# Kernel tuning notes

Measured on AMD Instinct MI355X. Metric: run time of the kernel, lower is better.

The kernel has to match this reference:

```python
import jax, jax.numpy as jnp
import numpy as np

B, C, W, H = 32, 256, 32, 32


def setup_inputs() -> dict:
    key = jax.random.key(0)
    ks = jax.random.split(key, 9)
    s = 1.0 / np.sqrt(C)
    return {
        "x": jax.random.normal(ks[0], (B, C, W, H), dtype=jnp.float32),
        "Wq": jax.random.normal(ks[1], (C, C), dtype=jnp.float32) * s,
        "bq": jax.random.normal(ks[2], (C,), dtype=jnp.float32) * 0.01,
        "Wk": jax.random.normal(ks[3], (C, C), dtype=jnp.float32) * s,
        "bk": jax.random.normal(ks[4], (C,), dtype=jnp.float32) * 0.01,
        "Wv": jax.random.normal(ks[5], (C, C), dtype=jnp.float32) * s,
        "bv": jax.random.normal(ks[6], (C,), dtype=jnp.float32) * 0.01,
        "rel_h": jax.random.normal(ks[7], (1, C, 1, H), dtype=jnp.float32),
        "rel_w": jax.random.normal(ks[8], (1, C, W, 1), dtype=jnp.float32),
    }


def reference(x, Wq, bq, Wk, bk, Wv, bv, rel_h, rel_w):
    b, c, w, h = x.shape
    n = w * h
    xf = x.reshape(b, c, n)  # [B, C, N]
    # 1x1 conv == channel-mixing matmul (out_ch 'o' from in_ch 'c')
    q = jnp.einsum('oc,bcn->bon', Wq, xf) + bq[None, :, None]
    k = jnp.einsum('oc,bcn->bon', Wk, xf) + bk[None, :, None]
    v = jnp.einsum('oc,bcn->bon', Wv, xf) + bv[None, :, None]
    # content-content: q^T k -> [B, N, N]
    content_content = jnp.einsum('bci,bcj->bij', q, k)
    # relative position bias: (rel_h + rel_w) broadcasts to [1, C, W, H]
    rel = (rel_h + rel_w).reshape(c, n)  # [C, N]
    content_position = jnp.einsum('cp,bcj->bpj', rel, q)  # [B, N, N]
    attention = jax.nn.softmax(content_content + content_position, axis=-1)
    # out[b,c,i] = sum_j v[b,c,j] * attention[b,i,j]
    out = jnp.einsum('bcj,bij->bci', v, attention)
    return out.reshape(b, c, w, h)
```

## Files before the change

### kernel.cpp

```cpp
#include <hip/hip_runtime.h>


#define NB 32
#define NC 256
#define NNN 1024

typedef _Float16 f16;
typedef __attribute__((ext_vector_type(8))) _Float16 half8;
typedef __attribute__((ext_vector_type(4))) float f32x4;
typedef __attribute__((ext_vector_type(4))) float float4v;

__device__ __forceinline__ f32x4 mfma16(half8 a, half8 b, f32x4 c) {
  return __builtin_amdgcn_mfma_f32_16x16x32_f16(a, b, c, 0, 0, 0);
}
__device__ __forceinline__ void gload16(const f16* g, f16* l) {
  __builtin_amdgcn_global_load_lds(
      (const __attribute__((address_space(1))) void*)g,
      (__attribute__((address_space(3))) void*)l, 16, 0, 0);
}

__global__ __launch_bounds__(256) void k_prep(
    const float* __restrict__ Wq, const float* __restrict__ Wk,
    const float* __restrict__ Wv, const float* __restrict__ relh,
    const float* __restrict__ relw, f16* __restrict__ Wh, f16* __restrict__ RT) {
  int bid = blockIdx.x, tid = threadIdx.x;
  if (bid < 192) {
    int base = (bid * 256 + tid) * 4;
    int w = base >> 16, j = base & 65535;
    const float* src = (w == 0) ? Wq : ((w == 1) ? Wk : Wv);
    float4v v = *(const float4v*)(src + j);
    Wh[base + 0] = (f16)v.x; Wh[base + 1] = (f16)v.y;
    Wh[base + 2] = (f16)v.z; Wh[base + 3] = (f16)v.w;
  } else {
    int n = bid - 192;
    int c = tid;
    RT[n * NC + c] = (f16)(relw[c * 32 + (n >> 5)] + relh[c * 32 + (n & 31)]);
  }
}

__global__ __launch_bounds__(256) void k_xpose(
    const float* __restrict__ x, f16* __restrict__ xT) {
  int bid = blockIdx.x;
  int nt = bid & 15, ct = (bid >> 4) & 3, b = bid >> 6;
  int c0 = ct << 6, n0 = nt << 6;
  __shared__ f16 T[64][72];
  int t = threadIdx.x;
  {
    int cl = t >> 2, n4 = (t & 3) << 4;
    const float* src = x + ((size_t)(b * NC + c0 + cl) << 10) + n0 + n4;
    float4v v0 = *(const float4v*)(src + 0);
    float4v v1 = *(const float4v*)(src + 4);
    float4v v2 = *(const float4v*)(src + 8);
    float4v v3 = *(const float4v*)(src + 12);
    f16* d = &T[cl][n4];
    d[0]=(f16)v0.x; d[1]=(f16)v0.y; d[2]=(f16)v0.z; d[3]=(f16)v0.w;
    d[4]=(f16)v1.x; d[5]=(f16)v1.y; d[6]=(f16)v1.z; d[7]=(f16)v1.w;
    d[8]=(f16)v2.x; d[9]=(f16)v2.y; d[10]=(f16)v2.z; d[11]=(f16)v2.w;
    d[12]=(f16)v3.x; d[13]=(f16)v3.y; d[14]=(f16)v3.z; d[15]=(f16)v3.w;
  }
  __syncthreads();
  {
    int nl = t >> 2, c16 = (t & 3) << 4;
    half8 h0, h1;
    #pragma unroll
    for (int u = 0; u < 8; ++u) h0[u] = T[c16 + u][nl];
    #pragma unroll
    for (int u = 0; u < 8; ++u) h1[u] = T[c16 + 8 + u][nl];
    f16* dst = xT + ((size_t)(b * NNN + n0 + nl) << 8) + c0 + c16;
    *(half8*)(dst) = h0;
    *(half8*)(dst + 8) = h1;
  }
}

__global__ __launch_bounds__(256, 2) void k_proj(
    const f16* __restrict__ xT, const f16* __restrict__ Wh,
    const float* __restrict__ bq, const float* __restrict__ bk,
    const float* __restrict__ bv,
    f16* __restrict__ KQ, f16* __restrict__ V) {
  int b = blockIdx.x >> 4;
  int n0 = (blockIdx.x & 15) << 6;
  int tid = threadIdx.x;
  int wave = tid >> 6, lane = tid & 63;
  int lq = lane & 15, g = lane >> 4;
  int ow = wave << 6;
  const f16* xTb = xT + ((size_t)(b * NNN + n0) << 8);

  __shared__ f16 XS[64][256];
  __shared__ f16 BB[18432];

  {
    int li = lane & 31;
    #pragma unroll
    for (int q2 = 0; q2 < 8; ++q2) {
      int r2 = wave * 16 + q2 * 2;
      int r = r2 + (lane >> 5);
      int slot = (li & 0x10) | ((li ^ (r & 15)) & 0xF);
      gload16(xTb + ((size_t)r << 8) + slot * 8, &XS[r2][0]);
    }
  }
  asm volatile("s_waitcnt vmcnt(0)" ::: "memory");
  __syncthreads();

  #pragma unroll 1
  for (int which = 0; which < 2; ++which) {
    const f16* Wp = Wh + which * 65536;
    const float* bias = which ? bk : bq;
    int koff = which ? 0 : 256;
    f32x4 acc[4][4];
    #pragma unroll
    for (int f = 0; f < 4; ++f) {
      float bf = bias[ow + 16 * f + lq];
      #pragma unroll
      for (int mm = 0; mm < 4; ++mm) acc[mm][f] = (f32x4){bf, bf, bf, bf};
    }
    #pragma unroll
    for (int kk = 0; kk < 8; ++kk) {
      int cb = kk * 32 + 8 * g;
      int s = 4 * kk + g;
      int p = (s & 0x10) | ((s ^ lq) & 0xF);
      half8 xa[4], wb[4];
      #pragma unroll
      for (int mm = 0; mm < 4; ++mm)
        xa[mm] = *(const half8*)(&XS[16 * mm + lq][p * 8]);
      #pragma unroll
      for (int f = 0; f < 4; ++f)
        wb[f] = *(const half8*)(Wp + (size_t)(ow + 16 * f + lq) * NC + cb);
      #pragma unroll
      for (int mm = 0; mm < 4; ++mm)
        #pragma unroll
        for (int f = 0; f < 4; ++f)
          acc[mm][f] = mfma16(xa[mm], wb[f], acc[mm][f]);
    }
    __syncthreads();
    #pragma unroll
    for (int mm = 0; mm < 4; ++mm)
      #pragma unroll
      for (int f = 0; f < 4; ++f)
        #pragma unroll
        for (int r = 0; r < 4; ++r)
          BB[(16 * mm + 4 * g + r) * 272 + ow + 16 * f + lq] = (f16)acc[mm][f][r];
    __syncthreads();
    #pragma unroll
    for (int it = 0; it < 8; ++it) {
      int row = wave * 16 + it * 2 + (lane >> 5);
      int cc = (lane & 31) * 8;
      half8 v = *(const half8*)(&BB[row * 272 + cc]);
      *(half8*)(&KQ[((size_t)(b * NNN + n0 + row) << 9) + koff + cc]) = v;
    }
  }

  {
    const f16* Wp = Wh + 2 * 65536;
    f32x4 acc[4][4];
    #pragma unroll
    for (int mm = 0; mm < 4; ++mm)
      #pragma unroll
      for (int r = 0; r < 4; ++r) {
        float bf = bv[ow + 16 * mm + 4 * g + r];
        #pragma unroll
        for (int f = 0; f < 4; ++f) acc[mm][f][r] = bf;
      }
    #pragma unroll
    for (int kk = 0; kk < 8; ++kk) {
      int cb = kk * 32 + 8 * g;
      int s = 4 * kk + g;
      int p = (s & 0x10) | ((s ^ lq) & 0xF);
      half8 va[4], xb2[4];
      #pragma unroll
      for (int mm = 0; mm < 4; ++mm)
        va[mm] = *(const half8*)(Wp + (size_t)(ow + 16 * mm + lq) * NC + cb);
      #pragma unroll
      for (int f = 0; f < 4; ++f)
        xb2[f] = *(const half8*)(&XS[16 * f + lq][p * 8]);
      #pragma unroll
      for (int mm = 0; mm < 4; ++mm)
        #pragma unroll
        for (int f = 0; f < 4; ++f)
          acc[mm][f] = mfma16(va[mm], xb2[f], acc[mm][f]);
    }
    __syncthreads();
    #pragma unroll
    for (int mm = 0; mm < 4; ++mm)
      #pragma unroll
      for (int f = 0; f < 4; ++f)
        #pragma unroll
        for (int r = 0; r < 4; ++r)
          BB[(ow + 16 * mm + 4 * g + r) * 72 + 16 * f + lq] = (f16)acc[mm][f][r];
    __syncthreads();
    #pragma unroll
    for (int it = 0; it < 8; ++it) {
      int o = wave * 64 + it * 8 + (lane >> 3);
      int cc = (lane & 7) * 8;
      half8 v = *(const half8*)(&BB[o * 72 + cc]);
      *(half8*)(&V[((size_t)(b * NC + o) << 10) + n0 + cc]) = v;
    }
  }
}

__global__ __launch_bounds__(256, 2) void k_flash6(
    const f16* __restrict__ KQ, const f16* __restrict__ V,
    const f16* __restrict__ RT, float* __restrict__ out) {
  int bid = blockIdx.x;
  int swz = (bid & 7) * 64 + (bid >> 3);
  int b = swz >> 4;
  int i0 = (swz & 15) << 6;
  int tid = threadIdx.x;
  int wave = tid >> 6, lane = tid & 63;
  int lq = lane & 15, g = lane >> 4;
  int iw = i0 + 16 * wave;

  __shared__ f16 KQS[2][2][16][512];

  const f16* KQb = KQ + ((size_t)b << 19);
  const f16* Vb = V + ((size_t)b << 18);

  half8 QA[16];
  #pragma unroll
  for (int kk = 0; kk < 8; ++kk)
    QA[kk] = *(const half8*)(KQb + ((size_t)(iw + lq) << 9) + 256 + kk * 32 + 8 * g);
  #pragma unroll
  for (int kk = 0; kk < 8; ++kk)
    QA[8 + kk] = *(const half8*)(RT + (size_t)(iw + lq) * NC + kk * 32 + 8 * g);

  f32x4 acc[16];
  #pragma unroll
  for (int cf = 0; cf < 16; ++cf) acc[cf] = (f32x4){0.f, 0.f, 0.f, 0.f};
  float m = -1e30f, lsum = 0.f;

#define STAGE(JT, BUF)                                                        \
  {                                                                           \
    _Pragma("unroll")                                                         \
    for (int pp = 0; pp < 2; ++pp) {                                          \
      _Pragma("unroll")                                                       \
      for (int q = 0; q < 4; ++q) {                                           \
        int rho_ = 4 * wave + q;                                              \
        int j_ = (JT) * 32 + 8 * wave + 4 * pp + q;                           \
        int slot_ = (lane & 0x30) | ((lane ^ rho_) & 0xF);                    \
        gload16(KQb + ((size_t)j_ << 9) + slot_ * 8, &KQS[BUF][pp][rho_][0]); \
      }                                                                       \
    }                                                                         \
  }

  STAGE(0, 0);
  asm volatile("s_waitcnt vmcnt(0)" ::: "memory");
  __syncthreads();

  #pragma unroll 1
  for (int jt = 0; jt < 32; ++jt) {
    int cur = jt & 1;
    if (jt < 31) {
      if (cur) STAGE(jt + 1, 0) else STAGE(jt + 1, 1);
    }
    f32x4 S0 = (f32x4){0.f, 0.f, 0.f, 0.f};
    f32x4 S1 = (f32x4){0.f, 0.f, 0.f, 0.f};
    const f16* B0 = &KQS[cur][0][lq][0];
    const f16* B1 = &KQS[cur][1][lq][0];
    __builtin_amdgcn_s_setprio(1);
    #pragma unroll
    for (int kk = 0; kk < 16; ++kk) {
      int s = 4 * kk + g;
      int ps = (s & 0x30) | ((s ^ lq) & 0xF);
      S0 = mfma16(*(const half8*)(B0 + ps * 8), QA[kk], S0);
      S1 = mfma16(*(const half8*)(B1 + ps * 8), QA[kk], S1);
    }
    __builtin_amdgcn_s_setprio(0);

    size_t j0 = (size_t)(jt * 32 + 8 * g);
    half8 vpre[8];
    #pragma unroll
    for (int cf = 0; cf < 8; ++cf)
      vpre[cf] = *(const half8*)(Vb + ((size_t)(16 * cf + lq) << 10) + j0);

    float pmax = fmaxf(fmaxf(fmaxf(S0[0], S0[1]), fmaxf(S0[2], S0[3])),
                       fmaxf(fmaxf(S1[0], S1[1]), fmaxf(S1[2], S1[3])));
    bool grow = pmax > m + 8.f;
    if (__builtin_amdgcn_ballot_w64(grow)) {
      float tmax = pmax;
      tmax = fmaxf(tmax, __shfl_xor(tmax, 16));
      tmax = fmaxf(tmax, __shfl_xor(tmax, 32));
      float mn = fmaxf(m, tmax);
      float sc = __expf(m - mn);
      m = mn;
      lsum *= sc;
      #pragma unroll
      for (int cf = 0; cf < 16; ++cf) {
        acc[cf][0] *= sc; acc[cf][1] *= sc; acc[cf][2] *= sc; acc[cf][3] *= sc;
      }
    }
    float p0 = __expf(S0[0] - m), p1 = __expf(S0[1] - m),
          p2 = __expf(S0[2] - m), p3 = __expf(S0[3] - m);
    float p4 = __expf(S1[0] - m), p5 = __expf(S1[1] - m),
          p6 = __expf(S1[2] - m), p7 = __expf(S1[3] - m);
    lsum += ((p0 + p1) + (p2 + p3)) + ((p4 + p5) + (p6 + p7));
    half8 pa;
    pa[0] = (f16)p0; pa[1] = (f16)p1; pa[2] = (f16)p2; pa[3] = (f16)p3;
    pa[4] = (f16)p4; pa[5] = (f16)p5; pa[6] = (f16)p6; pa[7] = (f16)p7;

    __builtin_amdgcn_s_setprio(1);
    #pragma unroll
    for (int cf = 0; cf < 8; ++cf)
      acc[cf] = mfma16(vpre[cf], pa, acc[cf]);
    #pragma unroll
    for (int cf = 8; cf < 16; ++cf) {
      half8 vv = *(const half8*)(Vb + ((size_t)(16 * cf + lq) << 10) + j0);
      acc[cf] = mfma16(vv, pa, acc[cf]);
    }
    __builtin_amdgcn_s_setprio(0);

    asm volatile("s_waitcnt vmcnt(0)" ::: "memory");
    __syncthreads();
  }
#undef STAGE

  lsum += __shfl_xor(lsum, 16);
  lsum += __shfl_xor(lsum, 32);
  float li = 1.f / lsum;
  #pragma unroll
  for (int cf = 0; cf < 16; ++cf)
    #pragma unroll
    for (int r = 0; r < 4; ++r)
      out[((size_t)(b * NC + 16 * cf + 4 * g + r) << 10) + iw + lq] = acc[cf][r] * li;
}

extern "C" void kernel_launch(void* const* d_in, const int* in_sizes, int n_in,
                              void* d_out, int out_size, void* d_ws, size_t ws_size,
                              hipStream_t stream) {
  const float* x = (const float*)d_in[0];
  const float* Wq = (const float*)d_in[1];
  const float* bq = (const float*)d_in[2];
  const float* Wk = (const float*)d_in[3];
  const float* bk = (const float*)d_in[4];
  const float* Wv = (const float*)d_in[5];
  const float* bv = (const float*)d_in[6];
  const float* relh = (const float*)d_in[7];
  const float* relw = (const float*)d_in[8];

  char* ws = (char*)d_ws;
  const size_t MB = 1 << 20;
  f16* xT = (f16*)(ws);
  f16* KQ = (f16*)(ws + 16 * MB);
  f16* V  = (f16*)(ws + 48 * MB);
  f16* RT = (f16*)(ws + 64 * MB);
  f16* Wh = (f16*)(ws + 64 * MB + 512 * 1024);

  k_prep<<<dim3(1216), dim3(256), 0, stream>>>(Wq, Wk, Wv, relh, relw, Wh, RT);
  k_xpose<<<dim3(2048), dim3(256), 0, stream>>>(x, xT);
  k_proj<<<dim3(512), dim3(256), 0, stream>>>(xT, Wh, bq, bk, bv, KQ, V);
  k_flash6<<<dim3(512), dim3(256), 0, stream>>>(KQ, V, RT, (float*)d_out);
}
```

Baseline: 327.4 us.

## Precompute content-position bias matrix in separate kernel, halve flash K dimension

Splits the concatenated KQ buffer into separate K and Q buffers and adds a kernel that materializes the full content-position term (rel^T q) as an fp16 B×N×N matrix. The flash kernel then runs QK^T with K-dimension 256 instead of 512, adds the precomputed bias tile loaded from global memory, and uses smaller LDS staging so it can target higher occupancy. The trade-off is writing and re-reading a 64 MB fp16 intermediate, which adds HBM traffic and fp16 rounding of the bias.

```diff
diff --git a/kernel.cpp b/kernel.cpp
--- a/kernel.cpp
+++ b/kernel.cpp
@@ -76,7 +76,7 @@
     const f16* __restrict__ xT, const f16* __restrict__ Wh,
     const float* __restrict__ bq, const float* __restrict__ bk,
     const float* __restrict__ bv,
-    f16* __restrict__ KQ, f16* __restrict__ V) {
+    f16* __restrict__ Km, f16* __restrict__ Qm, f16* __restrict__ V) {
   int b = blockIdx.x >> 4;
   int n0 = (blockIdx.x & 15) << 6;
   int tid = threadIdx.x;
@@ -105,7 +105,7 @@
   for (int which = 0; which < 2; ++which) {
     const f16* Wp = Wh + which * 65536;
     const float* bias = which ? bk : bq;
-    int koff = which ? 0 : 256;
+    f16* outp = which ? Km : Qm;
     f32x4 acc[4][4];
     #pragma unroll
     for (int f = 0; f < 4; ++f) {
@@ -145,7 +145,7 @@
       int row = wave * 16 + it * 2 + (lane >> 5);
       int cc = (lane & 31) * 8;
       half8 v = *(const half8*)(&BB[row * 272 + cc]);
-      *(half8*)(&KQ[((size_t)(b * NNN + n0 + row) << 9) + koff + cc]) = v;
+      *(half8*)(&outp[((size_t)(b * NNN + n0 + row) << 8) + cc]) = v;
     }
   }
 
@@ -197,9 +197,81 @@
   }
 }
 
-__global__ __launch_bounds__(256, 2) void k_flash6(
-    const f16* __restrict__ KQ, const f16* __restrict__ V,
-    const f16* __restrict__ RT, float* __restrict__ out) {
+__global__ __launch_bounds__(256, 2) void k_cp(
+    const f16* __restrict__ Qm, const f16* __restrict__ RT,
+    f16* __restrict__ CP) {
+  int b = blockIdx.x >> 4;
+  int j0 = (blockIdx.x & 15) << 6;
+  int tid = threadIdx.x;
+  int wave = tid >> 6, lane = tid & 63;
+  int lq = lane & 15, g = lane >> 4;
+
+  __shared__ f16 XS[64][256];
+  __shared__ f16 BB[4][64][72];
+
+  {
+    const f16* Qb = Qm + ((size_t)(b * NNN + j0) << 8);
+    int li = lane & 31;
+    #pragma unroll
+    for (int q2 = 0; q2 < 8; ++q2) {
+      int r2 = wave * 16 + q2 * 2;
+      int r = r2 + (lane >> 5);
+      int slot = (li & 0x10) | ((li ^ (r & 15)) & 0xF);
+      gload16(Qb + ((size_t)r << 8) + slot * 8, &XS[r2][0]);
+    }
+  }
+  asm volatile("s_waitcnt vmcnt(0)" ::: "memory");
+  __syncthreads();
+
+  #pragma unroll 1
+  for (int chunk = 0; chunk < 4; ++chunk) {
+    int i0c = wave * 256 + chunk * 64;
+    f32x4 acc[4][4];
+    #pragma unroll
+    for (int mm = 0; mm < 4; ++mm)
+      #pragma unroll
+      for (int f = 0; f < 4; ++f) acc[mm][f] = (f32x4){0.f, 0.f, 0.f, 0.f};
+    #pragma unroll
+    for (int kk = 0; kk < 8; ++kk) {
+      int cb = kk * 32 + 8 * g;
+      int s = 4 * kk + g;
+      int p = (s & 0x10) | ((s ^ lq) & 0xF);
+      half8 xa[4], wb[4];
+      #pragma unroll
+      for (int mm = 0; mm < 4; ++mm)
+        xa[mm] = *(const half8*)(&XS[16 * mm + lq][p * 8]);
+      #pragma unroll
+      for (int f = 0; f < 4; ++f)
+        wb[f] = *(const half8*)(RT + ((size_t)(i0c + 16 * f + lq) << 8) + cb);
+      #pragma unroll
+      for (int mm = 0; mm < 4; ++mm)
+        #pragma unroll
+        for (int f = 0; f < 4; ++f)
+          acc[mm][f] = mfma16(xa[mm], wb[f], acc[mm][f]);
+    }
+    #pragma unroll
+    for (int mm = 0; mm < 4; ++mm)
+      #pragma unroll
+      for (int f = 0; f < 4; ++f)
+        #pragma unroll
+        for (int r = 0; r < 4; ++r)
+          BB[wave][16 * f + lq][16 * mm + 4 * g + r] = (f16)acc[mm][f][r];
+    asm volatile("s_waitcnt lgkmcnt(0)" ::: "memory");
+    __builtin_amdgcn_sched_barrier(0);
+    const f16* bbr = &BB[wave][lane][0];
+    f16* dst = CP + ((size_t)((b << 10) + i0c + lane) << 10) + j0;
+    #pragma unroll
+    for (int jj = 0; jj < 8; ++jj) {
+      half8 h = *(const half8*)(bbr + jj * 8);
+      *(half8*)(dst + jj * 8) = h;
+    }
+  }
+}
+
+__global__ __launch_bounds__(256, 4) void k_flash7(
+    const f16* __restrict__ Km, const f16* __restrict__ Qm,
+    const f16* __restrict__ V, const f16* __restrict__ CP,
+    float* __restrict__ out) {
   int bid = blockIdx.x;
   int swz = (bid & 7) * 64 + (bid >> 3);
   int b = swz >> 4;
@@ -209,36 +281,33 @@
   int lq = lane & 15, g = lane >> 4;
   int iw = i0 + 16 * wave;
 
-  __shared__ f16 KQS[2][2][16][512];
-
-  const f16* KQb = KQ + ((size_t)b << 19);
+  __shared__ f16 KQS[2][2][16][256];
+
+  const f16* Kmb = Km + ((size_t)b << 18);
   const f16* Vb = V + ((size_t)b << 18);
-
-  half8 QA[16];
+  const f16* CPb = CP + ((size_t)((b << 10) + iw + lq) << 10);
+
+  half8 QA[8];
   #pragma unroll
   for (int kk = 0; kk < 8; ++kk)
-    QA[kk] = *(const half8*)(KQb + ((size_t)(iw + lq) << 9) + 256 + kk * 32 + 8 * g);
-  #pragma unroll
-  for (int kk = 0; kk < 8; ++kk)
-    QA[8 + kk] = *(const half8*)(RT + (size_t)(iw + lq) * NC + kk * 32 + 8 * g);
+    QA[kk] = *(const half8*)(Qm + ((size_t)(b * NNN + iw + lq) << 8) + kk * 32 + 8 * g);
 
   f32x4 acc[16];
   #pragma unroll
   for (int cf = 0; cf < 16; ++cf) acc[cf] = (f32x4){0.f, 0.f, 0.f, 0.f};
   float m = -1e30f, lsum = 0.f;
 
-#define STAGE(JT, BUF)                                                        \
-  {                                                                           \
-    _Pragma("unroll")                                                         \
-    for (int pp = 0; pp < 2; ++pp) {                                          \
-      _Pragma("unroll")                                                       \
-      for (int q = 0; q < 4; ++q) {                                           \
-        int rho_ = 4 * wave + q;                                              \
-        int j_ = (JT) * 32 + 8 * wave + 4 * pp + q;                           \
-        int slot_ = (lane & 0x30) | ((lane ^ rho_) & 0xF);                    \
-        gload16(KQb + ((size_t)j_ << 9) + slot_ * 8, &KQS[BUF][pp][rho_][0]); \
-      }                                                                       \
-    }                                                                         \
+#define STAGE(JT, BUF)                                                         \
+  {                                                                            \
+    _Pragma("unroll")                                                          \
+    for (int q = 0; q < 4; ++q) {                                              \
+      int gi_ = wave * 4 + q;                                                  \
+      int p_ = gi_ >> 3, rp_ = gi_ & 7;                                        \
+      int rho_ = 2 * rp_ + (lane >> 5);                                        \
+      int j_ = (JT) * 32 + 8 * (rho_ >> 2) + 4 * p_ + (rho_ & 3);              \
+      gload16(Kmb + ((size_t)j_ << 8) + (((lane & 31) ^ rho_) << 3),           \
+              &KQS[BUF][p_][2 * rp_][0]);                                      \
+    }                                                                          \
   }
 
   STAGE(0, 0);
@@ -257,27 +326,26 @@
     const f16* B1 = &KQS[cur][1][lq][0];
     __builtin_amdgcn_s_setprio(1);
     #pragma unroll
-    for (int kk = 0; kk < 16; ++kk) {
-      int s = 4 * kk + g;
-      int ps = (s & 0x30) | ((s ^ lq) & 0xF);
-      S0 = mfma16(*(const half8*)(B0 + ps * 8), QA[kk], S0);
-      S1 = mfma16(*(const half8*)(B1 + ps * 8), QA[kk], S1);
+    for (int kk = 0; kk < 8; ++kk) {
+      int ps = ((kk * 4 + g) ^ lq) << 3;
+      S0 = mfma16(*(const half8*)(B0 + ps), QA[kk], S0);
+      S1 = mfma16(*(const half8*)(B1 + ps), QA[kk], S1);
     }
     __builtin_amdgcn_s_setprio(0);
 
-    size_t j0 = (size_t)(jt * 32 + 8 * g);
-    half8 vpre[8];
-    #pragma unroll
-    for (int cf = 0; cf < 8; ++cf)
-      vpre[cf] = *(const half8*)(Vb + ((size_t)(16 * cf + lq) << 10) + j0);
-
-    float pmax = fmaxf(fmaxf(fmaxf(S0[0], S0[1]), fmaxf(S0[2], S0[3])),
+    half8 cp8 = *(const half8*)(CPb + jt * 32 + 8 * g);
+    #pragma unroll
+    for (int r = 0; r < 4; ++r) {
+      S0[r] += (float)cp8[r];
+      S1[r] += (float)cp8[4 + r];
+    }
+
+    float tmax = fmaxf(fmaxf(fmaxf(S0[0], S0[1]), fmaxf(S0[2], S0[3])),
                        fmaxf(fmaxf(S1[0], S1[1]), fmaxf(S1[2], S1[3])));
-    bool grow = pmax > m + 8.f;
+    tmax = fmaxf(tmax, __shfl_xor(tmax, 16));
+    tmax = fmaxf(tmax, __shfl_xor(tmax, 32));
+    bool grow = tmax > m + 8.f;
     if (__builtin_amdgcn_ballot_w64(grow)) {
-      float tmax = pmax;
-      tmax = fmaxf(tmax, __shfl_xor(tmax, 16));
-      tmax = fmaxf(tmax, __shfl_xor(tmax, 32));
       float mn = fmaxf(m, tmax);
       float sc = __expf(m - mn);
       m = mn;
@@ -296,12 +364,10 @@
     pa[0] = (f16)p0; pa[1] = (f16)p1; pa[2] = (f16)p2; pa[3] = (f16)p3;
     pa[4] = (f16)p4; pa[5] = (f16)p5; pa[6] = (f16)p6; pa[7] = (f16)p7;
 
+    size_t j0 = (size_t)(jt * 32 + 8 * g);
     __builtin_amdgcn_s_setprio(1);
     #pragma unroll
-    for (int cf = 0; cf < 8; ++cf)
-      acc[cf] = mfma16(vpre[cf], pa, acc[cf]);
-    #pragma unroll
-    for (int cf = 8; cf < 16; ++cf) {
+    for (int cf = 0; cf < 16; ++cf) {
       half8 vv = *(const half8*)(Vb + ((size_t)(16 * cf + lq) << 10) + j0);
       acc[cf] = mfma16(vv, pa, acc[cf]);
     }
@@ -337,14 +403,17 @@
 
   char* ws = (char*)d_ws;
   const size_t MB = 1 << 20;
+  f16* CP = (f16*)(ws);
   f16* xT = (f16*)(ws);
-  f16* KQ = (f16*)(ws + 16 * MB);
-  f16* V  = (f16*)(ws + 48 * MB);
-  f16* RT = (f16*)(ws + 64 * MB);
-  f16* Wh = (f16*)(ws + 64 * MB + 512 * 1024);
+  f16* Km = (f16*)(ws + 64 * MB);
+  f16* Qm = (f16*)(ws + 80 * MB);
+  f16* V  = (f16*)(ws + 96 * MB);
+  f16* RT = (f16*)(ws + 112 * MB);
+  f16* Wh = (f16*)(ws + 112 * MB + 512 * 1024);
 
   k_prep<<<dim3(1216), dim3(256), 0, stream>>>(Wq, Wk, Wv, relh, relw, Wh, RT);
   k_xpose<<<dim3(2048), dim3(256), 0, stream>>>(x, xT);
-  k_proj<<<dim3(512), dim3(256), 0, stream>>>(xT, Wh, bq, bk, bv, KQ, V);
-  k_flash6<<<dim3(512), dim3(256), 0, stream>>>(KQ, V, RT, (float*)d_out);
-}
+  k_proj<<<dim3(512), dim3(256), 0, stream>>>(xT, Wh, bq, bk, bv, Km, Qm, V);
+  k_cp<<<dim3(512), dim3(256), 0, stream>>>(Qm, RT, CP);
+  k_flash7<<<dim3(512), dim3(256), 0, stream>>>(Km, Qm, V, CP, (float*)d_out);
+}
```

Result: slower. 417.4 us (+27.5%).
